# Kernel optimization log

Hardware: AMD Instinct MI355X
Metric: run time of the kernel (lower is better)

## Reference

```python
import jax, jax.numpy as jnp
import numpy as np

LN_EPS = 1e-5

def _layernorm(z, g, b):
    m = jnp.mean(z, axis=-1, keepdims=True)
    v = jnp.mean(jnp.square(z - m), axis=-1, keepdims=True)
    return (z - m) / jnp.sqrt(v + LN_EPS) * g + b

def setup_inputs() -> dict:
    key = jax.random.key(0)
    ks = jax.random.split(key, 8)
    B, N, C, H = 16, 1024, 384, 6
    Dff = 4 * C
    s = 0.02
    return {
        "x": jax.random.normal(ks[0], (B, N, C), dtype=jnp.float32),
        "ln1_g": jnp.ones((C,), jnp.float32),
        "ln1_b": jnp.zeros((C,), jnp.float32),
        "qkv_w": jax.random.normal(ks[1], (3 * C, C), jnp.float32) * s,
        "proj_w": jax.random.normal(ks[2], (C, C), jnp.float32) * s,
        "proj_b": jnp.zeros((C,), jnp.float32),
        "gate_h": jnp.ones((H,), jnp.float32),
        "ln2_g": jnp.ones((C,), jnp.float32),
        "ln2_b": jnp.zeros((C,), jnp.float32),
        "fc1_w": jax.random.normal(ks[3], (Dff, C), jnp.float32) * s,
        "fc1_b": jnp.zeros((Dff,), jnp.float32),
        "fc2_w": jax.random.normal(ks[4], (C, Dff), jnp.float32) * s,
        "fc2_b": jnp.zeros((C,), jnp.float32),
        "gate_mlp": jnp.ones((Dff,), jnp.float32),
    }

def reference(x, ln1_g, ln1_b, qkv_w, proj_w, proj_b, gate_h,
              ln2_g, ln2_b, fc1_w, fc1_b, fc2_w, fc2_b, gate_mlp):
    B, N, C = x.shape
    H = gate_h.shape[0]
    Dh = C // H
    scale = Dh ** -0.5

    # Attention branch
    h = _layernorm(x, ln1_g, ln1_b)
    qkv = (h @ qkv_w.T).reshape(B, N, 3, H, Dh).transpose(2, 0, 3, 1, 4)  # [3,B,H,N,Dh]
    q, k, v = qkv[0], qkv[1], qkv[2]
    attn = jax.nn.softmax(jnp.einsum('bhnd,bhmd->bhnm', q, k) * scale, axis=-1)  # [B,H,N,N]
    o = jnp.einsum('bhnm,bhmd->bhnd', attn, v)            # [B,H,N,Dh]
    o = o.transpose(0, 2, 1, 3) * gate_h[None, None, :, None]  # per-head gate
    o = o.reshape(B, N, C) @ proj_w.T + proj_b
    x = x + o

    # MLP branch (exact GELU, per-neuron gate)
    h2 = _layernorm(x, ln2_g, ln2_b)
    m = jax.nn.gelu(h2 @ fc1_w.T + fc1_b, approximate=False) * gate_mlp
    x = x + (m @ fc2_w.T + fc2_b)
    return x
```

## Files before the change

### kernel.cpp

```cpp
#include <hip/hip_runtime.h>
#include <hip/hip_bf16.h>
#include <cstdint>
#include <cstddef>

#define B_   16
#define N_   1024
#define C_   384
#define H_   6
#define DFF_ 1536
#define R_   16384

typedef __attribute__((ext_vector_type(8))) __bf16 bf16x8;
typedef __attribute__((ext_vector_type(4))) float  f32x4;
typedef __attribute__((ext_vector_type(8))) unsigned short u16x8;
typedef __attribute__((ext_vector_type(4))) unsigned short u16x4;

__device__ __forceinline__ float bf2f(unsigned short u){
    unsigned int x = ((unsigned int)u) << 16;
    return __builtin_bit_cast(float, x);
}
__device__ __forceinline__ unsigned short f2bf(float f){
    return __builtin_bit_cast(unsigned short, __float2bfloat16(f));
}
__device__ __forceinline__ unsigned int cvt_pk_bf16(float a, float b){
    unsigned int r;
    asm("v_cvt_pk_bf16_f32 %0, %1, %2" : "=v"(r) : "v"(a), "v"(b));
    return r;
}
__device__ __forceinline__ float fast_exp2(float x){
    float r;
    asm("v_exp_f32 %0, %1" : "=v"(r) : "v"(x));
    return r;
}
__device__ __forceinline__ void gload16(const void* g, void* l){
    __builtin_amdgcn_global_load_lds(
        (const __attribute__((address_space(1))) unsigned int*)g,
        (__attribute__((address_space(3))) unsigned int*)l, 16, 0, 0);
}
__device__ __forceinline__ float gelu_f(float u){
    float z  = fabsf(u) * 0.70710678118654752f;
    float t  = __builtin_amdgcn_rcpf(1.0f + 0.47047f*z);
    float e  = __expf(-z*z);
    float p  = t*(0.3480242f + t*(-0.0958798f + t*0.7478556f));
    float er = 1.0f - p*e;
    return 0.5f*u*(1.0f + copysignf(er, u));
}
__device__ __forceinline__ float ldv(const float* p, size_t i){ return p[i]; }
__device__ __forceinline__ float ldv(const __hip_bfloat16* p, size_t i){ return __bfloat162float(p[i]); }

__global__ __launch_bounds__(256) void ln1_cvt_kernel(
    const float* __restrict__ x, const float* __restrict__ g,
    const float* __restrict__ b, __hip_bfloat16* __restrict__ out,
    const float* __restrict__ i0, __hip_bfloat16* __restrict__ o0, int n0,
    const float* __restrict__ i1, __hip_bfloat16* __restrict__ o1, int n1,
    const float* __restrict__ i2, __hip_bfloat16* __restrict__ o2, int n2,
    const float* __restrict__ i3, __hip_bfloat16* __restrict__ o3, int n3)
{
    if (blockIdx.x < 4096){
        const int lane = threadIdx.x & 63;
        const int wave = threadIdx.x >> 6;
        const int row  = blockIdx.x*4 + wave;
        const float* xr = x + (size_t)row*C_;
        float v[6];
        float s = 0.f;
        #pragma unroll
        for (int i=0;i<6;i++){ v[i] = xr[lane + i*64]; s += v[i]; }
        #pragma unroll
        for (int m=1;m<64;m<<=1) s += __shfl_xor(s, m);
        const float mean = s * (1.0f/C_);
        float sq = 0.f;
        #pragma unroll
        for (int i=0;i<6;i++){ float d = v[i]-mean; sq += d*d; }
        #pragma unroll
        for (int m=1;m<64;m<<=1) sq += __shfl_xor(sq, m);
        const float rstd = rsqrtf(sq*(1.0f/C_) + 1e-5f);
        #pragma unroll
        for (int i=0;i<6;i++){
            int c = lane + i*64;
            out[(size_t)row*C_ + c] = __float2bfloat16((v[i]-mean)*rstd*g[c] + b[c]);
        }
    } else {
        const int total = n0+n1+n2+n3;
        for (int i = (blockIdx.x-4096)*blockDim.x + threadIdx.x; i < total; i += 1024*blockDim.x){
            int k = i;
            if (k < n0){ o0[k] = __float2bfloat16(i0[k]); continue; }
            k -= n0;
            if (k < n1){ o1[k] = __float2bfloat16(i1[k]); continue; }
            k -= n1;
            if (k < n2){ o2[k] = __float2bfloat16(i2[k]); continue; }
            k -= n2;
            o3[k] = __float2bfloat16(i3[k]);
        }
    }
}

template<typename T>
__global__ __launch_bounds__(256) void ln_kernel(
    const T* __restrict__ x, const float* __restrict__ g,
    const float* __restrict__ b, __hip_bfloat16* __restrict__ out)
{
    const int lane = threadIdx.x & 63;
    const int wave = threadIdx.x >> 6;
    const int row  = blockIdx.x*4 + wave;
    const T* xr = x + (size_t)row*C_;
    float v[6];
    float s = 0.f;
    #pragma unroll
    for (int i=0;i<6;i++){ v[i] = ldv(xr, lane + i*64); s += v[i]; }
    #pragma unroll
    for (int m=1;m<64;m<<=1) s += __shfl_xor(s, m);
    const float mean = s * (1.0f/C_);
    float sq = 0.f;
    #pragma unroll
    for (int i=0;i<6;i++){ float d = v[i]-mean; sq += d*d; }
    #pragma unroll
    for (int m=1;m<64;m<<=1) sq += __shfl_xor(sq, m);
    const float rstd = rsqrtf(sq*(1.0f/C_) + 1e-5f);
    #pragma unroll
    for (int i=0;i<6;i++){
        int c = lane + i*64;
        out[(size_t)row*C_ + c] = __float2bfloat16((v[i]-mean)*rstd*g[c] + b[c]);
    }
}

#define BK2 32
enum { EPI_QKV=0, EPI_PROJ=1, EPI_FC1=2, EPI_FC2=3 };

template<int EPI, int BMt, int BNt, int NBUF, int MW, int NTH>
__global__ __launch_bounds__(NTH, MW) void gemm_bt(
    const __hip_bfloat16* __restrict__ A,
    const __hip_bfloat16* __restrict__ W,
    const int M, const int N, const int K,
    const float* __restrict__ bias,
    const float* __restrict__ resid,
    const __hip_bfloat16* __restrict__ residb,
    const float* __restrict__ gate,
    float* __restrict__ outf,
    __hip_bfloat16* __restrict__ outb)
{
    constexpr int NWAVE = NTH/64;
    constexpr int NWC   = (BNt >= 128) ? 2 : 1;
    constexpr int NWR   = NWAVE/NWC;
    constexpr int WRS   = BMt/NWR;
    constexpr int MI    = WRS/16;
    constexpr int APASS = (BMt*BK2*2)/(NTH*16);
    constexpr int BPASS = (BNt*BK2*2)/(NTH*16);
    constexpr int LPT   = APASS + BPASS;
    constexpr int RPP   = NTH/4;
    __shared__ __align__(16) unsigned short As[NBUF][BMt*BK2];
    __shared__ __align__(16) unsigned short Bs[NBUF][BNt*BK2];
    const int t = threadIdx.x;
    const int l = t & 63;
    const int w = t >> 6;
    const int wr = (NWC==2) ? (w >> 1) : w;
    const int wc = (NWC==2) ? (w & 1)  : 0;
    const int nb = N / BNt;
    const int rbX = (M/BMt) >> 3;
    const int X  = blockIdx.x & 7;
    const int j8 = blockIdx.x >> 3;
    const int rb = X*rbX + j8 / nb;
    const int cb = j8 % nb;
    const int srow2 = t >> 2;
    const int sgcol = (((t&3) - ((t>>3)&3)) & 3) * 8;
    f32x4 acc[MI][4];
    #pragma unroll
    for (int i=0;i<MI;i++)
        #pragma unroll
        for (int jj=0;jj<4;jj++) acc[i][jj] = (f32x4){0.f,0.f,0.f,0.f};

    const size_t arow0 = (size_t)rb*BMt + srow2;
    const size_t brow0 = (size_t)cb*BNt + srow2;

    auto STAGE = [&](int buf, int k0){
        #pragma unroll
        for (int c=0;c<APASS;c++)
            gload16(A + (arow0 + c*RPP)*K + k0 + sgcol, (char*)&As[buf][0] + c*(NTH*16) + t*16);
        #pragma unroll
        for (int c=0;c<BPASS;c++)
            gload16(W + (brow0 + c*RPP)*K + k0 + sgcol, (char*)&Bs[buf][0] + c*(NTH*16) + t*16);
    };

    auto COMPUTE = [&](int buf){
        const char* as = (const char*)&As[buf][0];
        const char* bs = (const char*)&Bs[buf][0];
        bf16x8 af[MI], bw[4];
        #pragma unroll
        for (int i=0;i<MI;i++){
            const int r = wr*WRS + i*16 + (l&15);
            const int sl = ((l>>4) + ((r>>1)&3)) & 3;
            af[i] = *(const bf16x8*)(as + r*64 + sl*16);
        }
        #pragma unroll
        for (int i=0;i<4;i++){
            const int r = wc*64 + i*16 + (l&15);
            const int sl = ((l>>4) + ((r>>1)&3)) & 3;
            bw[i] = *(const bf16x8*)(bs + r*64 + sl*16);
        }
        #pragma unroll
        for (int mi=0;mi<MI;mi++)
            #pragma unroll
            for (int ni=0;ni<4;ni++)
                acc[mi][ni] = __builtin_amdgcn_mfma_f32_16x16x32_bf16(af[mi], bw[ni], acc[mi][ni], 0,0,0);
    };

    const int nst = K/BK2;
    if constexpr (NBUF==2){
        STAGE(0, 0);
        for (int s=0; s<nst; ++s){
            asm volatile("s_waitcnt vmcnt(0)" ::: "memory");
            __builtin_amdgcn_s_barrier();
            asm volatile("" ::: "memory");
            if (s+1 < nst) STAGE((s+1)&1, (s+1)*BK2);
            COMPUTE(s&1);
        }
    } else {
        STAGE(0, 0);
        STAGE(1, BK2);
        int cur = 0, stb = 2;
        for (int s=0; s<nst; ++s){
            if (s < nst-1){
                if constexpr (LPT==4) asm volatile("s_waitcnt vmcnt(4)" ::: "memory");
                else                  asm volatile("s_waitcnt vmcnt(3)" ::: "memory");
            } else {
                asm volatile("s_waitcnt vmcnt(0)" ::: "memory");
            }
            __builtin_amdgcn_s_barrier();
            asm volatile("" ::: "memory");
            if (s+2 < nst){
                STAGE(stb, (s+2)*BK2);
                stb = (stb+1==3) ? 0 : stb+1;
            }
            COMPUTE(cur);
            cur = (cur+1==3) ? 0 : cur+1;
        }
    }
    const int rowBase = rb*BMt + wr*WRS;
    const int colBase = cb*BNt + wc*64;
    #pragma unroll
    for (int ni=0; ni<4; ni++){
        const int col = colBase + ni*16 + (l&15);
        #pragma unroll
        for (int mi=0; mi<MI; mi++){
            #pragma unroll
            for (int jj=0;jj<4;jj++){
                const int row = rowBase + mi*16 + (l>>4)*4 + jj;
                const float vx = acc[mi][ni][jj];
                size_t idx = (size_t)row*N + col;
                if constexpr (EPI==EPI_PROJ){
                    outb[idx] = __float2bfloat16(resid[idx] + vx + bias[col]);
                } else if constexpr (EPI==EPI_FC2){
                    outf[idx] = bf2f(*((const unsigned short*)residb + idx)) + vx + bias[col];
                } else {
                    outb[idx] = __float2bfloat16(gelu_f(vx + bias[col]) * gate[col]);
                }
            }
        }
    }
}


template<int EPI, int NCOLS>
__global__ __launch_bounds__(256, 2) void gemm_wres(
    const __hip_bfloat16* __restrict__ A,
    const __hip_bfloat16* __restrict__ Wt,
    const float* __restrict__ bias,
    const float* __restrict__ resid,
    const float* __restrict__ gate,
    __hip_bfloat16* __restrict__ outb)
{
    constexpr int NB = NCOLS/64;
    constexpr int G  = 24;
    __shared__ __align__(16) unsigned short As[4][128*32];
    __shared__ __align__(16) unsigned short Bs[64*384];
    const int t = threadIdx.x;
    const int l = t & 63;
    const int w = t >> 6;
    const int X  = blockIdx.x & 7;
    const int j8 = blockIdx.x >> 3;
    const int rb = X*8 + j8 / NB;
    const int cb = j8 % NB;

    #pragma unroll
    for (int j=0;j<12;j++){
        const int L     = (w*12 + j)*1024 + l*16;
        const int row   = L / 768;
        const int cbyte = L - row*768;
        const int scol  = (cbyte ^ ((row&7)<<4)) >> 1;
        gload16(Wt + (size_t)(cb*64 + row)*384 + scol, (char*)&Bs[0] + L);
    }
    const int sgcol = (((l&3) - ((l>>3)&3)) & 3) * 8;
    const size_t arow0 = (size_t)rb*256 + w*32 + (l>>2);
    auto STAGEA = [&](int g){
        const int rt = g/12, s = g - rt*12;
        #pragma unroll
        for (int c=0;c<2;c++)
            gload16(A + (arow0 + rt*128 + c*16)*384 + s*32 + sgcol,
                    (char*)&As[g&3][0] + w*2048 + c*1024 + l*16);
    };
    STAGEA(0); STAGEA(1); STAGEA(2);
    asm volatile("s_waitcnt vmcnt(6)" ::: "memory");
    __builtin_amdgcn_s_barrier();

    #pragma unroll
    for (int rt=0; rt<2; ++rt){
        f32x4 acc[2][4];
        #pragma unroll
        for (int i=0;i<2;i++)
            #pragma unroll
            for (int jj=0;jj<4;jj++) acc[i][jj] = (f32x4){0.f,0.f,0.f,0.f};

        #pragma unroll
        for (int s=0; s<12; ++s){
            const int g = rt*12 + s;
            if (g <= G-3)      asm volatile("s_waitcnt vmcnt(4)" ::: "memory");
            else if (g == G-2) asm volatile("s_waitcnt vmcnt(2)" ::: "memory");
            else               asm volatile("s_waitcnt vmcnt(0)" ::: "memory");
            const char* as = (const char*)&As[g&3][0] + w*2048;
            bf16x8 af[2], bw[4];
            #pragma unroll
            for (int i=0;i<2;i++){
                const int r  = i*16 + (l&15);
                const int sl = ((l>>4) + ((r>>1)&3)) & 3;
                af[i] = *(const bf16x8*)(as + r*64 + sl*16);
            }
            #pragma unroll
            for (int i=0;i<4;i++){
                const int r = i*16 + (l&15);
                bw[i] = *(const bf16x8*)((const char*)&Bs[0] + r*768
                             + ((s*64 + (l>>4)*16) ^ ((r&7)<<4)));
            }
            #pragma unroll
            for (int mi=0;mi<2;mi++)
                #pragma unroll
                for (int ni=0;ni<4;ni++)
                    acc[mi][ni] = __builtin_amdgcn_mfma_f32_16x16x32_bf16(af[mi], bw[ni], acc[mi][ni], 0,0,0);
            asm volatile("s_waitcnt lgkmcnt(0)" ::: "memory");
            if (g+3 < G) STAGEA(g+3);
        }
        const int rowBase = rb*256 + rt*128 + w*32;
        if constexpr (EPI==EPI_QKV){
            unsigned short* ob = (unsigned short*)outb;
            #pragma unroll
            for (int ni=0; ni<4; ni++){
                const int col = cb*64 + ni*16 + (l&15);
                const int p = col/384, rem = col - p*384;
                const int hh = rem>>6, d = rem&63;
                #pragma unroll
                for (int mi=0; mi<2; mi++){
                    const int row0 = rowBase + mi*16 + (l>>4)*4;
                    const int bb = row0>>10, n = row0&1023;
                    if (p==2){
                        u16x4 pk;
                        #pragma unroll
                        for (int jj=0;jj<4;jj++) pk[jj] = f2bf(acc[mi][ni][jj]);
                        *(u16x4*)(ob + (size_t)2*6291456 + ((size_t)(bb*H_+hh)*64 + d)*1024 + n) = pk;
                    } else {
                        #pragma unroll
                        for (int jj=0;jj<4;jj++)
                            ob[(((size_t)((p*16+bb)*6+hh))<<16) + ((size_t)(n+jj)<<6) + d] = f2bf(acc[mi][ni][jj]);
                    }
                }
            }
        } else {
            #pragma unroll
            for (int ni=0; ni<4; ni++){
                const int col = cb*64 + ni*16 + (l&15);
                #pragma unroll
                for (int mi=0; mi<2; mi++){
                    #pragma unroll
                    for (int jj=0;jj<4;jj++){
                        const int row = rowBase + mi*16 + (l>>4)*4 + jj;
                        const size_t idx = (size_t)row*NCOLS + col;
                        if constexpr (EPI==EPI_PROJ){
                            outb[idx] = __float2bfloat16(resid[idx] + acc[mi][ni][jj] + bias[col]);
                        } else {
                            outb[idx] = __float2bfloat16(gelu_f(acc[mi][ni][jj] + bias[col]) * gate[col]);
                        }
                    }
                }
            }
        }
    }
}

template<int EPI, int NCOLS>
__global__ __launch_bounds__(256, 2) void gemm_wres4(
    const __hip_bfloat16* __restrict__ A,
    const __hip_bfloat16* __restrict__ Wt,
    const float* __restrict__ bias,
    const float* __restrict__ resid,
    const float* __restrict__ gate,
    __hip_bfloat16* __restrict__ outb)
{
    constexpr int NB = NCOLS/64;
    __shared__ __align__(16) unsigned short As[4][128*32];
    __shared__ __align__(16) unsigned short Bs[64*384];
    const int t = threadIdx.x;
    const int l = t & 63;
    const int w = t >> 6;
    const int X  = blockIdx.x & 7;
    const int j8 = blockIdx.x >> 3;
    const int rb = X*16 + j8 / NB;
    const int cb = j8 % NB;

    #pragma unroll
    for (int j=0;j<12;j++){
        const int L     = (w*12 + j)*1024 + l*16;
        const int row   = L / 768;
        const int cbyte = L - row*768;
        const int scol  = (cbyte ^ ((row&7)<<4)) >> 1;
        gload16(Wt + (size_t)(cb*64 + row)*384 + scol, (char*)&Bs[0] + L);
    }
    const int sgcol = (((l&3) - ((l>>3)&3)) & 3) * 8;
    const size_t arow0 = (size_t)rb*128 + w*32 + (l>>2);
    auto STAGEA = [&](int g){
        #pragma unroll
        for (int c=0;c<2;c++)
            gload16(A + (arow0 + c*16)*384 + g*32 + sgcol,
                    (char*)&As[g&3][0] + w*2048 + c*1024 + l*16);
    };
    STAGEA(0); STAGEA(1); STAGEA(2);
    asm volatile("s_waitcnt vmcnt(6)" ::: "memory");
    __builtin_amdgcn_s_barrier();

    f32x4 acc[2][4];
    #pragma unroll
    for (int i=0;i<2;i++)
        #pragma unroll
        for (int jj=0;jj<4;jj++) acc[i][jj] = (f32x4){0.f,0.f,0.f,0.f};

    #pragma unroll
    for (int s=0; s<12; ++s){
        if (s < 10)      asm volatile("s_waitcnt vmcnt(4)" ::: "memory");
        else if (s == 10) asm volatile("s_waitcnt vmcnt(2)" ::: "memory");
        else              asm volatile("s_waitcnt vmcnt(0)" ::: "memory");
        const char* as = (const char*)&As[s&3][0] + w*2048;
        bf16x8 af[2], bw[4];
        #pragma unroll
        for (int i=0;i<2;i++){
            const int r  = i*16 + (l&15);
            const int sl = ((l>>4) + ((r>>1)&3)) & 3;
            af[i] = *(const bf16x8*)(as + r*64 + sl*16);
        }
        #pragma unroll
        for (int i=0;i<4;i++){
            const int r = i*16 + (l&15);
            bw[i] = *(const bf16x8*)((const char*)&Bs[0] + r*768
                         + ((s*64 + (l>>4)*16) ^ ((r&7)<<4)));
        }
        #pragma unroll
        for (int mi=0;mi<2;mi++)
            #pragma unroll
            for (int ni=0;ni<4;ni++)
                acc[mi][ni] = __builtin_amdgcn_mfma_f32_16x16x32_bf16(af[mi], bw[ni], acc[mi][ni], 0,0,0);
        asm volatile("s_waitcnt lgkmcnt(0)" ::: "memory");
        if (s+3 < 12) STAGEA(s+3);
    }

    const int rowBase = rb*128 + w*32;
    #pragma unroll
    for (int ni=0; ni<4; ni++){
        const int col = cb*64 + ni*16 + (l&15);
        #pragma unroll
        for (int mi=0; mi<2; mi++){
            #pragma unroll
            for (int jj=0;jj<4;jj++){
                const int row = rowBase + mi*16 + (l>>4)*4 + jj;
                const size_t idx = (size_t)row*NCOLS + col;
                if constexpr (EPI==EPI_PROJ){
                    outb[idx] = __float2bfloat16(resid[idx] + acc[mi][ni][jj] + bias[col]);
                } else {
                    outb[idx] = __float2bfloat16(gelu_f(acc[mi][ni][jj] + bias[col]) * gate[col]);
                }
            }
        }
    }
}

__global__ __launch_bounds__(256) void attn_mfma(
    const __hip_bfloat16* __restrict__ qg,
    const __hip_bfloat16* __restrict__ kg,
    const __hip_bfloat16* __restrict__ vtg,
    const float* __restrict__ gate_h,
    __hip_bfloat16* __restrict__ og)
{
    __shared__ __align__(16) unsigned short Ks [3][64*64];
    __shared__ __align__(16) unsigned short Vts[3][64*64];
    const int t = threadIdx.x;
    const int l = t & 63;
    const int w = t >> 6;
    const int X  = blockIdx.x & 7;
    const int j8 = blockIdx.x >> 3;
    const int bh = X*12 + (j8 >> 3);
    const int n0 = (j8 & 7) * 128;
    const int h  = bh % H_;
    const int b  = bh / H_;
    const unsigned short* qp  = (const unsigned short*)qg  + ((size_t)bh*N_ + n0 + w*32)*64;
    const unsigned short* kp  = (const unsigned short*)kg  + (size_t)bh*N_*64;
    const unsigned short* vtp = (const unsigned short*)vtg + (size_t)bh*64*N_;

    bf16x8 qf[2][2];
    #pragma unroll
    for (int mt=0;mt<2;mt++)
        #pragma unroll
        for (int dc=0;dc<2;dc++){
            u16x8 raw = *(const u16x8*)(qp + ((size_t)(mt*16 + (l&15)))*64 + dc*32 + (l>>4)*8);
            u16x8 sc;
            #pragma unroll
            for (int j=0;j<8;j++) sc[j] = f2bf(bf2f(raw[j]) * 0.1803368801111244f);
            qf[mt][dc] = __builtin_bit_cast(bf16x8, sc);
        }

    int qk_off[4][2], pv_off[2][4];
    #pragma unroll
    for (int t4=0;t4<4;t4++){
        const int i    = l & 15;
        const int row  = 8*(i>>2) + (i&3) + 4*(t4&1) + 32*(t4>>1);
        const int swzr = (row&3) | (((row>>3)&1)<<2);
        #pragma unroll
        for (int dc=0;dc<2;dc++)
            qk_off[t4][dc] = row*128 + ((dc*64 + (l>>4)*16) ^ (swzr<<4));
    }
    #pragma unroll
    for (int nt=0;nt<4;nt++){
        const int row  = nt*16 + (l&15);
        const int swzr = (row&3) | (((row>>3)&1)<<2);
        #pragma unroll
        for (int kc=0;kc<2;kc++)
            pv_off[kc][nt] = row*128 + ((kc*64 + (l>>4)*16) ^ (swzr<<4));
    }

    const int sr  = t >> 3;
    const int sce = (t & 7) * 8;

    auto STAGE = [&](int buf, int kt){
        #pragma unroll
        for (int c=0;c<2;c++){
            const int r    = sr + c*32;
            const int swzr = (r&3) | (((r>>3)&1)<<2);
            const int col  = sce ^ (swzr<<3);
            gload16(kp  + ((size_t)(kt*64 + r))*64 + col, (char*)&Ks [buf][0] + (c*256 + t)*16);
            gload16(vtp + (size_t)r*N_ + kt*64 + col,     (char*)&Vts[buf][0] + (c*256 + t)*16);
        }
    };

    f32x4 o_acc[2][4];
    #pragma unroll
    for (int i=0;i<2;i++)
        #pragma unroll
        for (int jj=0;jj<4;jj++) o_acc[i][jj] = (f32x4){0.f,0.f,0.f,0.f};
    float rs_part[2] = {0.f, 0.f};

    STAGE(0, 0);
    STAGE(1, 1);
    int cur = 0, stb = 2;
    for (int kt=0; kt<16; kt++){
        if (kt < 15) asm volatile("s_waitcnt vmcnt(4)" ::: "memory");
        else         asm volatile("s_waitcnt vmcnt(0)" ::: "memory");
        __builtin_amdgcn_s_barrier();
        asm volatile("" ::: "memory");
        if (kt < 14){
            STAGE(stb, kt+2);
            stb = (stb+1==3) ? 0 : stb+1;
        }
        const char* ks = (const char*)&Ks[cur][0];
        const char* vs = (const char*)&Vts[cur][0];

        f32x4 s_acc[4][2];
        #pragma unroll
        for (int i=0;i<4;i++)
            #pragma unroll
            for (int jj=0;jj<2;jj++) s_acc[i][jj] = (f32x4){0.f,0.f,0.f,0.f};
        #pragma unroll
        for (int t4=0;t4<4;t4++)
            #pragma unroll
            for (int dc=0;dc<2;dc++){
                bf16x8 kf = *(const bf16x8*)(ks + qk_off[t4][dc]);
                #pragma unroll
                for (int mt=0;mt<2;mt++)
                    s_acc[t4][mt] = __builtin_amdgcn_mfma_f32_16x16x32_bf16(kf, qf[mt][dc], s_acc[t4][mt], 0,0,0);
            }
        #pragma unroll
        for (int mt=0;mt<2;mt++){
            float acc_s = 0.f;
            #pragma unroll
            for (int t4=0;t4<4;t4++){
                #pragma unroll
                for (int jj=0;jj<4;jj++){
                    float e = fast_exp2(s_acc[t4][mt][jj]);
                    s_acc[t4][mt][jj] = e;
                    acc_s += e;
                }
            }
            rs_part[mt] += acc_s;
        }
        #pragma unroll
        for (int kc=0;kc<2;kc++){
            union { unsigned int u[4]; bf16x8 v; } pu[2];
            #pragma unroll
            for (int mt=0;mt<2;mt++){
                pu[mt].u[0] = cvt_pk_bf16(s_acc[2*kc  ][mt][0], s_acc[2*kc  ][mt][1]);
                pu[mt].u[1] = cvt_pk_bf16(s_acc[2*kc  ][mt][2], s_acc[2*kc  ][mt][3]);
                pu[mt].u[2] = cvt_pk_bf16(s_acc[2*kc+1][mt][0], s_acc[2*kc+1][mt][1]);
                pu[mt].u[3] = cvt_pk_bf16(s_acc[2*kc+1][mt][2], s_acc[2*kc+1][mt][3]);
            }
            #pragma unroll
            for (int nt=0;nt<4;nt++){
                bf16x8 vf = *(const bf16x8*)(vs + pv_off[kc][nt]);
                #pragma unroll
                for (int mt=0;mt<2;mt++)
                    o_acc[mt][nt] = __builtin_amdgcn_mfma_f32_16x16x32_bf16(pu[mt].v, vf, o_acc[mt][nt], 0,0,0);
            }
        }
        cur = (cur+1==3) ? 0 : cur+1;
    }
    float rowsum[2];
    #pragma unroll
    for (int mt=0;mt<2;mt++){
        float rs = rs_part[mt];
        rs += __shfl_xor(rs, 16);
        rs += __shfl_xor(rs, 32);
        rowsum[mt] = rs;
    }
    const float gh = gate_h[h];
    float inv[2][4];
    #pragma unroll
    for (int mt=0;mt<2;mt++)
        #pragma unroll
        for (int r=0;r<4;r++)
            inv[mt][r] = gh / __shfl(rowsum[mt], (l>>4)*4 + r, 16);
    unsigned short* op = (unsigned short*)og + ((size_t)b*N_ + n0 + w*32)*C_ + h*64;
    #pragma unroll
    for (int mt=0;mt<2;mt++){
        #pragma unroll
        for (int r=0;r<4;r++){
            const int n = mt*16 + (l>>4)*4 + r;
            #pragma unroll
            for (int nt=0;nt<4;nt++)
                op[(size_t)n*C_ + nt*16 + (l&15)] = f2bf(o_acc[mt][nt][r]*inv[mt][r]);
        }
    }
}

extern "C" void kernel_launch(void* const* d_in, const int* in_sizes, int n_in,
                              void* d_out, int out_size, void* d_ws, size_t ws_size,
                              hipStream_t stream)
{
    const float* x     = (const float*)d_in[0];
    const float* ln1g  = (const float*)d_in[1];
    const float* ln1b  = (const float*)d_in[2];
    const float* qkvw  = (const float*)d_in[3];
    const float* projw = (const float*)d_in[4];
    const float* projb = (const float*)d_in[5];
    const float* gateh = (const float*)d_in[6];
    const float* ln2g  = (const float*)d_in[7];
    const float* ln2b  = (const float*)d_in[8];
    const float* fc1w  = (const float*)d_in[9];
    const float* fc1b  = (const float*)d_in[10];
    const float* fc2w  = (const float*)d_in[11];
    const float* fc2b  = (const float*)d_in[12];
    const float* gatem = (const float*)d_in[13];
    float* out = (float*)d_out;

    char* ws = (char*)d_ws;
    __hip_bfloat16* h_buf = (__hip_bfloat16*)(ws + 0);
    __hip_bfloat16* qkv   = (__hip_bfloat16*)(ws + 12582912);
    __hip_bfloat16* q_buf = qkv;
    __hip_bfloat16* k_buf = qkv + 6291456;
    __hip_bfloat16* vt_buf= qkv + 2*6291456;
    __hip_bfloat16* o_buf = (__hip_bfloat16*)(ws + 50331648);
    __hip_bfloat16* m_buf = (__hip_bfloat16*)(ws + 12582912);
    __hip_bfloat16* x1b   = (__hip_bfloat16*)(ws + 62914560);
    __hip_bfloat16* wqkv  = (__hip_bfloat16*)(ws + 88080384);
    __hip_bfloat16* wproj = (__hip_bfloat16*)(ws + 88965120);
    __hip_bfloat16* wfc1  = (__hip_bfloat16*)(ws + 89260032);
    __hip_bfloat16* wfc2  = (__hip_bfloat16*)(ws + 90439680);

    ln1_cvt_kernel<<<5120, 256, 0, stream>>>(x, ln1g, ln1b, h_buf,
                                             qkvw, wqkv, 1152*384,
                                             projw, wproj, 384*384,
                                             fc1w, wfc1, 1536*384,
                                             fc2w, wfc2, 384*1536);

    gemm_wres<EPI_QKV,1152><<<1152, 256, 0, stream>>>(h_buf, wqkv, nullptr, nullptr, nullptr, qkv);
    attn_mfma<<<768, 256, 0, stream>>>(q_buf, k_buf, vt_buf, gateh, o_buf);
    gemm_wres<EPI_PROJ,384><<<384, 256, 0, stream>>>(o_buf, wproj, projb, x, nullptr, x1b);
    ln_kernel<__hip_bfloat16><<<4096, 256, 0, stream>>>(x1b, ln2g, ln2b, h_buf);
    gemm_wres4<EPI_FC1,1536><<<3072, 256, 0, stream>>>(h_buf, wfc1, fc1b, nullptr, gatem, m_buf);
    gemm_bt<EPI_FC2,64,128,3,1,256><<<768, 256, 0, stream>>>(m_buf, wfc2, R_, 384, 1536,
                                                             fc2b, nullptr, x1b, nullptr, out, nullptr);
}
```

Before: 173.7 us.

## Replace FC2 generic GEMM with weight-resident streaming kernel over K quarters

Swaps the generic triple-buffered gemm_bt used for FC2 for a specialized kernel with a 128x64 output tile. It holds a 64x384 slice of the FC2 weight in shared memory and reloads it four times across K=1536, while A tiles stream through a four-deep ring with fine-grained vmcnt waits. The aim is to cut redundant weight staging and barrier overhead per K step, following the weight-resident pattern already used by the other GEMMs. The cost is a full barrier and refill stall at each weight-quarter boundary, and the removed gemm_bt template plus simplified epilogues are cleanup.

```diff
diff --git a/kernel.cpp b/kernel.cpp
--- a/kernel.cpp
+++ b/kernel.cpp
@@ -123,140 +123,7 @@
     }
 }
 
-#define BK2 32
-enum { EPI_QKV=0, EPI_PROJ=1, EPI_FC1=2, EPI_FC2=3 };
-
-template<int EPI, int BMt, int BNt, int NBUF, int MW, int NTH>
-__global__ __launch_bounds__(NTH, MW) void gemm_bt(
-    const __hip_bfloat16* __restrict__ A,
-    const __hip_bfloat16* __restrict__ W,
-    const int M, const int N, const int K,
-    const float* __restrict__ bias,
-    const float* __restrict__ resid,
-    const __hip_bfloat16* __restrict__ residb,
-    const float* __restrict__ gate,
-    float* __restrict__ outf,
-    __hip_bfloat16* __restrict__ outb)
-{
-    constexpr int NWAVE = NTH/64;
-    constexpr int NWC   = (BNt >= 128) ? 2 : 1;
-    constexpr int NWR   = NWAVE/NWC;
-    constexpr int WRS   = BMt/NWR;
-    constexpr int MI    = WRS/16;
-    constexpr int APASS = (BMt*BK2*2)/(NTH*16);
-    constexpr int BPASS = (BNt*BK2*2)/(NTH*16);
-    constexpr int LPT   = APASS + BPASS;
-    constexpr int RPP   = NTH/4;
-    __shared__ __align__(16) unsigned short As[NBUF][BMt*BK2];
-    __shared__ __align__(16) unsigned short Bs[NBUF][BNt*BK2];
-    const int t = threadIdx.x;
-    const int l = t & 63;
-    const int w = t >> 6;
-    const int wr = (NWC==2) ? (w >> 1) : w;
-    const int wc = (NWC==2) ? (w & 1)  : 0;
-    const int nb = N / BNt;
-    const int rbX = (M/BMt) >> 3;
-    const int X  = blockIdx.x & 7;
-    const int j8 = blockIdx.x >> 3;
-    const int rb = X*rbX + j8 / nb;
-    const int cb = j8 % nb;
-    const int srow2 = t >> 2;
-    const int sgcol = (((t&3) - ((t>>3)&3)) & 3) * 8;
-    f32x4 acc[MI][4];
-    #pragma unroll
-    for (int i=0;i<MI;i++)
-        #pragma unroll
-        for (int jj=0;jj<4;jj++) acc[i][jj] = (f32x4){0.f,0.f,0.f,0.f};
-
-    const size_t arow0 = (size_t)rb*BMt + srow2;
-    const size_t brow0 = (size_t)cb*BNt + srow2;
-
-    auto STAGE = [&](int buf, int k0){
-        #pragma unroll
-        for (int c=0;c<APASS;c++)
-            gload16(A + (arow0 + c*RPP)*K + k0 + sgcol, (char*)&As[buf][0] + c*(NTH*16) + t*16);
-        #pragma unroll
-        for (int c=0;c<BPASS;c++)
-            gload16(W + (brow0 + c*RPP)*K + k0 + sgcol, (char*)&Bs[buf][0] + c*(NTH*16) + t*16);
-    };
-
-    auto COMPUTE = [&](int buf){
-        const char* as = (const char*)&As[buf][0];
-        const char* bs = (const char*)&Bs[buf][0];
-        bf16x8 af[MI], bw[4];
-        #pragma unroll
-        for (int i=0;i<MI;i++){
-            const int r = wr*WRS + i*16 + (l&15);
-            const int sl = ((l>>4) + ((r>>1)&3)) & 3;
-            af[i] = *(const bf16x8*)(as + r*64 + sl*16);
-        }
-        #pragma unroll
-        for (int i=0;i<4;i++){
-            const int r = wc*64 + i*16 + (l&15);
-            const int sl = ((l>>4) + ((r>>1)&3)) & 3;
-            bw[i] = *(const bf16x8*)(bs + r*64 + sl*16);
-        }
-        #pragma unroll
-        for (int mi=0;mi<MI;mi++)
-            #pragma unroll
-            for (int ni=0;ni<4;ni++)
-                acc[mi][ni] = __builtin_amdgcn_mfma_f32_16x16x32_bf16(af[mi], bw[ni], acc[mi][ni], 0,0,0);
-    };
-
-    const int nst = K/BK2;
-    if constexpr (NBUF==2){
-        STAGE(0, 0);
-        for (int s=0; s<nst; ++s){
-            asm volatile("s_waitcnt vmcnt(0)" ::: "memory");
-            __builtin_amdgcn_s_barrier();
-            asm volatile("" ::: "memory");
-            if (s+1 < nst) STAGE((s+1)&1, (s+1)*BK2);
-            COMPUTE(s&1);
-        }
-    } else {
-        STAGE(0, 0);
-        STAGE(1, BK2);
-        int cur = 0, stb = 2;
-        for (int s=0; s<nst; ++s){
-            if (s < nst-1){
-                if constexpr (LPT==4) asm volatile("s_waitcnt vmcnt(4)" ::: "memory");
-                else                  asm volatile("s_waitcnt vmcnt(3)" ::: "memory");
-            } else {
-                asm volatile("s_waitcnt vmcnt(0)" ::: "memory");
-            }
-            __builtin_amdgcn_s_barrier();
-            asm volatile("" ::: "memory");
-            if (s+2 < nst){
-                STAGE(stb, (s+2)*BK2);
-                stb = (stb+1==3) ? 0 : stb+1;
-            }
-            COMPUTE(cur);
-            cur = (cur+1==3) ? 0 : cur+1;
-        }
-    }
-    const int rowBase = rb*BMt + wr*WRS;
-    const int colBase = cb*BNt + wc*64;
-    #pragma unroll
-    for (int ni=0; ni<4; ni++){
-        const int col = colBase + ni*16 + (l&15);
-        #pragma unroll
-        for (int mi=0; mi<MI; mi++){
-            #pragma unroll
-            for (int jj=0;jj<4;jj++){
-                const int row = rowBase + mi*16 + (l>>4)*4 + jj;
-                const float vx = acc[mi][ni][jj];
-                size_t idx = (size_t)row*N + col;
-                if constexpr (EPI==EPI_PROJ){
-                    outb[idx] = __float2bfloat16(resid[idx] + vx + bias[col]);
-                } else if constexpr (EPI==EPI_FC2){
-                    outf[idx] = bf2f(*((const unsigned short*)residb + idx)) + vx + bias[col];
-                } else {
-                    outb[idx] = __float2bfloat16(gelu_f(vx + bias[col]) * gate[col]);
-                }
-            }
-        }
-    }
-}
+enum { EPI_QKV=0, EPI_PROJ=1, EPI_FC2=3 };
 
 
 template<int EPI, int NCOLS>
@@ -371,11 +238,7 @@
                     for (int jj=0;jj<4;jj++){
                         const int row = rowBase + mi*16 + (l>>4)*4 + jj;
                         const size_t idx = (size_t)row*NCOLS + col;
-                        if constexpr (EPI==EPI_PROJ){
-                            outb[idx] = __float2bfloat16(resid[idx] + acc[mi][ni][jj] + bias[col]);
-                        } else {
-                            outb[idx] = __float2bfloat16(gelu_f(acc[mi][ni][jj] + bias[col]) * gate[col]);
-                        }
+                        outb[idx] = __float2bfloat16(resid[idx] + acc[mi][ni][jj] + bias[col]);
                     }
                 }
             }
@@ -383,12 +246,11 @@
     }
 }
 
-template<int EPI, int NCOLS>
+template<int NCOLS>
 __global__ __launch_bounds__(256, 2) void gemm_wres4(
     const __hip_bfloat16* __restrict__ A,
     const __hip_bfloat16* __restrict__ Wt,
     const float* __restrict__ bias,
-    const float* __restrict__ resid,
     const float* __restrict__ gate,
     __hip_bfloat16* __restrict__ outb)
 {
@@ -467,11 +329,116 @@
             for (int jj=0;jj<4;jj++){
                 const int row = rowBase + mi*16 + (l>>4)*4 + jj;
                 const size_t idx = (size_t)row*NCOLS + col;
-                if constexpr (EPI==EPI_PROJ){
-                    outb[idx] = __float2bfloat16(resid[idx] + acc[mi][ni][jj] + bias[col]);
-                } else {
-                    outb[idx] = __float2bfloat16(gelu_f(acc[mi][ni][jj] + bias[col]) * gate[col]);
-                }
+                outb[idx] = __float2bfloat16(gelu_f(acc[mi][ni][jj] + bias[col]) * gate[col]);
+            }
+        }
+    }
+}
+
+__global__ __launch_bounds__(256, 2) void gemm_wres_fc2(
+    const __hip_bfloat16* __restrict__ A,
+    const __hip_bfloat16* __restrict__ Wt,
+    const float* __restrict__ bias,
+    const __hip_bfloat16* __restrict__ residb,
+    float* __restrict__ outf)
+{
+    constexpr int NB = 6;
+    __shared__ __align__(16) unsigned short As[4][128*32];
+    __shared__ __align__(16) unsigned short Bs[64*384];
+    const int t = threadIdx.x;
+    const int l = t & 63;
+    const int w = t >> 6;
+    const int X  = blockIdx.x & 7;
+    const int j8 = blockIdx.x >> 3;
+    const int rb = X*16 + j8 / NB;
+    const int cb = j8 % NB;
+
+    auto STAGEB = [&](int q){
+        #pragma unroll
+        for (int j=0;j<12;j++){
+            const int L     = (w*12 + j)*1024 + l*16;
+            const int row   = L / 768;
+            const int cbyte = L - row*768;
+            const int scol  = (cbyte ^ ((row&7)<<4)) >> 1;
+            gload16(Wt + (size_t)(cb*64 + row)*1536 + q*384 + scol, (char*)&Bs[0] + L);
+        }
+    };
+    const int sgcol = (((l&3) - ((l>>3)&3)) & 3) * 8;
+    const size_t arow0 = (size_t)rb*128 + w*32 + (l>>2);
+    auto STAGEA = [&](int g){
+        #pragma unroll
+        for (int c=0;c<2;c++)
+            gload16(A + (arow0 + c*16)*1536 + g*32 + sgcol,
+                    (char*)&As[g&3][0] + w*2048 + c*1024 + l*16);
+    };
+
+    STAGEB(0);
+    STAGEA(0); STAGEA(1); STAGEA(2);
+    asm volatile("s_waitcnt vmcnt(0)" ::: "memory");
+    __builtin_amdgcn_s_barrier();
+    asm volatile("" ::: "memory");
+
+    f32x4 acc[2][4];
+    #pragma unroll
+    for (int i=0;i<2;i++)
+        #pragma unroll
+        for (int jj=0;jj<4;jj++) acc[i][jj] = (f32x4){0.f,0.f,0.f,0.f};
+
+    for (int q=0; q<4; ++q){
+        if (q > 0){
+            asm volatile("s_waitcnt vmcnt(0)" ::: "memory");
+            __builtin_amdgcn_s_barrier();
+            asm volatile("" ::: "memory");
+        }
+        #pragma unroll
+        for (int s=0; s<12; ++s){
+            const int g = q*12 + s;
+            if (s >= 3){
+                if (g < 46)      asm volatile("s_waitcnt vmcnt(4)" ::: "memory");
+                else if (g == 46) asm volatile("s_waitcnt vmcnt(2)" ::: "memory");
+                else              asm volatile("s_waitcnt vmcnt(0)" ::: "memory");
+            }
+            const char* as = (const char*)&As[g&3][0] + w*2048;
+            bf16x8 af[2], bw[4];
+            #pragma unroll
+            for (int i=0;i<2;i++){
+                const int r  = i*16 + (l&15);
+                const int sl = ((l>>4) + ((r>>1)&3)) & 3;
+                af[i] = *(const bf16x8*)(as + r*64 + sl*16);
+            }
+            #pragma unroll
+            for (int i=0;i<4;i++){
+                const int r = i*16 + (l&15);
+                bw[i] = *(const bf16x8*)((const char*)&Bs[0] + r*768
+                             + ((s*64 + (l>>4)*16) ^ ((r&7)<<4)));
+            }
+            #pragma unroll
+            for (int mi=0;mi<2;mi++)
+                #pragma unroll
+                for (int ni=0;ni<4;ni++)
+                    acc[mi][ni] = __builtin_amdgcn_mfma_f32_16x16x32_bf16(af[mi], bw[ni], acc[mi][ni], 0,0,0);
+            asm volatile("s_waitcnt lgkmcnt(0)" ::: "memory");
+            if (g+3 < 48) STAGEA(g+3);
+        }
+        if (q < 3){
+            __builtin_amdgcn_s_barrier();
+            asm volatile("" ::: "memory");
+            STAGEB(q+1);
+        }
+    }
+
+    const int rowBase = rb*128 + w*32;
+    const unsigned short* xb = (const unsigned short*)residb;
+    #pragma unroll
+    for (int ni=0; ni<4; ni++){
+        const int col = cb*64 + ni*16 + (l&15);
+        #pragma unroll
+        for (int mi=0; mi<2; mi++){
+            #pragma unroll
+            for (int jj=0;jj<4;jj++){
+                const int row = rowBase + mi*16 + (l>>4)*4 + jj;
+                const size_t idx = (size_t)row*384 + col;
+                outf[idx] = bf2f(xb[idx]) + acc[mi][ni][jj] + bias[col];
             }
         }
     }
@@ -686,7 +653,6 @@
     attn_mfma<<<768, 256, 0, stream>>>(q_buf, k_buf, vt_buf, gateh, o_buf);
     gemm_wres<EPI_PROJ,384><<<384, 256, 0, stream>>>(o_buf, wproj, projb, x, nullptr, x1b);
     ln_kernel<__hip_bfloat16><<<4096, 256, 0, stream>>>(x1b, ln2g, ln2b, h_buf);
-    gemm_wres4<EPI_FC1,1536><<<3072, 256, 0, stream>>>(h_buf, wfc1, fc1b, nullptr, gatem, m_buf);
-    gemm_bt<EPI_FC2,64,128,3,1,256><<<768, 256, 0, stream>>>(m_buf, wfc2, R_, 384, 1536,
-                                                             fc2b, nullptr, x1b, nullptr, out, nullptr);
-}
+    gemm_wres4<1536><<<3072, 256, 0, stream>>>(h_buf, wfc1, fc1b, gatem, m_buf);
+    gemm_wres_fc2<<<768, 256, 0, stream>>>(m_buf, wfc2, fc2b, x1b, out);
+}
```

Measured after the change: 169.3 us. 2.5% less time.
